# Kernel optimization log

Measured on AMD Instinct MI355X. Metric: run time of the kernel, lower is better.

Reference implementation:

```python
import jax, jax.numpy as jnp
import numpy as np

B, S, H, D = 2, 2048, 16, 64
DM = H * D  # d_model = 1024


def setup_inputs() -> dict:
    key = jax.random.key(0)
    ks = jax.random.split(key, 12)
    scale = 1.0 / np.sqrt(DM)
    inp = {
        "queries": jax.random.normal(ks[0], (B, S, DM), jnp.float32),
        "keys": jax.random.normal(ks[1], (B, S, DM), jnp.float32),
        "values": jax.random.normal(ks[2], (B, S, DM), jnp.float32),
        # binary (0/1) causal mask, broadcast to (B, H, S, S) as the torch API expects
        "mask": jnp.broadcast_to(jnp.tril(jnp.ones((S, S), jnp.float32)), (B, H, S, S)),
        "wq": jax.random.normal(ks[3], (DM, DM), jnp.float32) * scale,
        "bq": jax.random.normal(ks[4], (DM,), jnp.float32) * scale,
        "wk": jax.random.normal(ks[5], (DM, DM), jnp.float32) * scale,
        "bk": jax.random.normal(ks[6], (DM,), jnp.float32) * scale,
        "wv": jax.random.normal(ks[7], (DM, DM), jnp.float32) * scale,
        "bv": jax.random.normal(ks[8], (DM,), jnp.float32) * scale,
        "wy": jax.random.normal(ks[9], (DM, DM), jnp.float32) * scale,
        "by": jax.random.normal(ks[10], (DM,), jnp.float32) * scale,
    }
    return inp


def _split_heads(x):
    # (B, S, H*D) -> (B, H, S, D)
    b, s, _ = x.shape
    return x.reshape(b, s, H, D).transpose(0, 2, 1, 3)


def reference(queries, keys, values, mask, wq, bq, wk, bk, wv, bv, wy, by):
    # torch nn.Linear: y = x @ W^T + b
    q = _split_heads(queries @ wq.T + bq)  # (B, H, S, D)
    k = _split_heads(keys @ wk.T + bk)
    v = _split_heads(values @ wv.T + bv)

    s = jnp.einsum("bhqd,bhkd->bhqk", q, k) / jnp.sqrt(jnp.float32(D))
    # custom additive-multiplicative mask: s*mask - 1e4*(1-mask)
    s = s * mask - 1e4 * (1.0 - mask)
    w = jax.nn.softmax(s, axis=-1)
    av = jnp.einsum("bhqk,bhkd->bhqd", w, v)  # (B, H, S, D)
    y = av.transpose(0, 2, 1, 3).reshape(queries.shape[0], queries.shape[1], DM)
    return y @ wy.T + by
```

## Files before the change

kernel.cpp:

```cpp
#include <hip/hip_runtime.h>
#include <math.h>

#define BB 2
#define SS 2048
#define HH 16
#define DD 64
#define DMODEL 1024
#define MROWS (BB * SS)

typedef __attribute__((ext_vector_type(8))) short bf16x8;
typedef __attribute__((ext_vector_type(4))) float f32x4;

__device__ __forceinline__ f32x4 mfma16(bf16x8 a, bf16x8 b, f32x4 c) {
    return __builtin_amdgcn_mfma_f32_16x16x32_bf16(a, b, c, 0, 0, 0);
}

__device__ __forceinline__ unsigned short bf16_1(float x) {
    unsigned u = __builtin_bit_cast(unsigned, x);
    u += 0x7fffu + ((u >> 16) & 1u);
    return (unsigned short)(u >> 16);
}
__device__ __forceinline__ unsigned pack_bf16(float a, float b) {
    unsigned ua = __builtin_bit_cast(unsigned, a);
    unsigned ub = __builtin_bit_cast(unsigned, b);
    ua += 0x7fffu + ((ua >> 16) & 1u);
    ub += 0x7fffu + ((ub >> 16) & 1u);
    return (ua >> 16) | (ub & 0xffff0000u);
}

__global__ __launch_bounds__(256) void cvt_bf16(const float* __restrict__ q,
                                                const float* __restrict__ k,
                                                const float* __restrict__ v,
                                                const float* __restrict__ wq,
                                                const float* __restrict__ wk,
                                                const float* __restrict__ wv,
                                                const float* __restrict__ wy,
                                                unsigned short* __restrict__ dst)
{
    const size_t idx = ((size_t)blockIdx.x * 256 + threadIdx.x) * 8;
    const int mc = (int)(idx >> 20);
    const float* src; size_t off;
    if      (mc < 4)   { src = q;  off = idx; }
    else if (mc < 8)   { src = k;  off = idx - ((size_t)4  << 20); }
    else if (mc < 12)  { src = v;  off = idx - ((size_t)8  << 20); }
    else if (mc == 12) { src = wq; off = idx - ((size_t)12 << 20); }
    else if (mc == 13) { src = wk; off = idx - ((size_t)13 << 20); }
    else if (mc == 14) { src = wv; off = idx - ((size_t)14 << 20); }
    else               { src = wy; off = idx - ((size_t)15 << 20); }
    float4 a = *(const float4*)(src + off);
    float4 b = *(const float4*)(src + off + 4);
    uint4 o;
    o.x = pack_bf16(a.x, a.y); o.y = pack_bf16(a.z, a.w);
    o.z = pack_bf16(b.x, b.y); o.w = pack_bf16(b.z, b.w);
    *(uint4*)(dst + idx) = o;
}

__global__ __launch_bounds__(256) void gemm_mfma(const unsigned short* __restrict__ A,
                                                 const unsigned short* __restrict__ W,
                                                 const float* __restrict__ bias,
                                                 void* __restrict__ out,
                                                 int a_mode, int out_mode)
{
    __shared__ int4 lds4[2048];
    const int tid = threadIdx.x;
    const int w   = tid >> 6;
    const int lane = tid & 63;
    const int L = lane & 15, Q = lane >> 4;
    const int m0 = blockIdx.x * 128;
    const int n0 = blockIdx.y * 128;
    const int wm = (w & 1) * 64;
    const int wn = (w >> 1) * 64;

    f32x4 acc[4][4] = {};

    for (int c = 0; c < 16; ++c) {
        __syncthreads();
        #pragma unroll
        for (int i = 0; i < 4; ++i) {
            int cid = tid + 256 * i;
            int row = cid >> 3, ch = cid & 7;
            int m = m0 + row;
            size_t gaddr;
            if (a_mode == 0) gaddr = (size_t)m * DMODEL + (size_t)c * 64 + ch * 8;
            else {
                int b = m >> 11, s = m & 2047;
                gaddr = (((size_t)b * HH + c) * SS + s) * DD + ch * 8;
            }
            int4 val = *(const int4*)(A + gaddr);
            lds4[row * 8 + (ch ^ (row & 7))] = val;
        }
        #pragma unroll
        for (int i = 0; i < 4; ++i) {
            int cid = tid + 256 * i;
            int row = cid >> 3, ch = cid & 7;
            int4 val = *(const int4*)(W + (size_t)(n0 + row) * DMODEL + (size_t)c * 64 + ch * 8);
            lds4[1024 + row * 8 + (ch ^ (row & 7))] = val;
        }
        __syncthreads();
        #pragma unroll
        for (int kf = 0; kf < 2; ++kf) {
            bf16x8 af[4], bfr[4];
            #pragma unroll
            for (int mt = 0; mt < 4; ++mt) {
                int row = wm + 16 * mt + L;
                af[mt] = __builtin_bit_cast(bf16x8, lds4[row * 8 + ((Q + 4 * kf) ^ (L & 7))]);
            }
            #pragma unroll
            for (int nt = 0; nt < 4; ++nt) {
                int row = wn + 16 * nt + L;
                bfr[nt] = __builtin_bit_cast(bf16x8, lds4[1024 + row * 8 + ((Q + 4 * kf) ^ (L & 7))]);
            }
            #pragma unroll
            for (int mt = 0; mt < 4; ++mt)
                #pragma unroll
                for (int nt = 0; nt < 4; ++nt)
                    acc[mt][nt] = mfma16(af[mt], bfr[nt], acc[mt][nt]);
        }
    }

    #pragma unroll
    for (int mt = 0; mt < 4; ++mt)
        #pragma unroll
        for (int nt = 0; nt < 4; ++nt)
            #pragma unroll
            for (int r = 0; r < 4; ++r) {
                int m = m0 + wm + 16 * mt + 4 * Q + r;
                int n = n0 + wn + 16 * nt + L;
                float val = acc[mt][nt][r] + bias[n];
                if (out_mode == 0) {
                    int b = m >> 11, s = m & 2047, h = n >> 6, d = n & 63;
                    ((unsigned short*)out)[(((size_t)b * HH + h) * SS + s) * DD + d] = bf16_1(val);
                } else {
                    ((float*)out)[(size_t)m * DMODEL + n] = val;
                }
            }
}

__global__ __launch_bounds__(256) void attn_mfma(const unsigned short* __restrict__ qb,
                                                 const unsigned short* __restrict__ kb,
                                                 const unsigned short* __restrict__ vb,
                                                 unsigned short* __restrict__ av)
{
    __shared__ int4 lds4[2048];
    const int tid  = threadIdx.x;
    const int w    = tid >> 6;
    const int lane = tid & 63;
    const int L = lane & 15, Q = lane >> 4;
    const int h = blockIdx.y, b = blockIdx.z;
    const size_t base = ((size_t)b * HH + h) * SS * DD;
    const float SC = 0.125f * 1.4426950408889634f;

    const int srcA = L + 32 * (Q & 1);
    const int srcB = srcA + 16;

    for (int pass = 0; pass < 2; ++pass) {
        const int qt  = pass ? (15 - (int)blockIdx.x) : (int)blockIdx.x;
        const int q0  = qt * 128;
        const int q0w = q0 + 32 * w;

        __syncthreads();
        #pragma unroll
        for (int i = 0; i < 4; ++i) {
            int cid = tid + 256 * i;
            int row = cid >> 3, ch = cid & 7;
            int4 val = *(const int4*)(qb + base + (size_t)(q0 + row) * DD + ch * 8);
            lds4[row * 8 + (ch ^ (row & 7))] = val;
        }
        __syncthreads();

        bf16x8 qf[2][2];
        #pragma unroll
        for (int ct = 0; ct < 2; ++ct)
            #pragma unroll
            for (int kf = 0; kf < 2; ++kf) {
                int row = 32 * w + 16 * ct + L;
                qf[ct][kf] = __builtin_bit_cast(bf16x8, lds4[row * 8 + ((Q + 4 * kf) ^ (L & 7))]);
            }

        float m2[2] = {-1e30f, -1e30f};
        float l2[2] = {0.f, 0.f};
        f32x4 acc[4][2] = {};

        const int nkt   = 2 * qt + 2;
        const int qmaxw = q0w + 31;
        for (int kt = 0; kt < nkt; ++kt) {
            const int k0 = kt * 64;
            __syncthreads();
            #pragma unroll
            for (int i = 0; i < 2; ++i) {
                int cid = tid + 256 * i;
                int row = cid >> 3, ch = cid & 7;
                int4 val = *(const int4*)(kb + base + (size_t)(k0 + row) * DD + ch * 8);
                lds4[1024 + row * 8 + (ch ^ (row & 7))] = val;
            }
            {
                int r4 = tid >> 4, c4 = tid & 15;
                uint2 rv[4];
                #pragma unroll
                for (int i = 0; i < 4; ++i)
                    rv[i] = *(const uint2*)(vb + base + (size_t)(k0 + r4 * 4 + i) * DD + c4 * 4);
                uint2* vt2 = (uint2*)(lds4 + 1536);
                #pragma unroll
                for (int j = 0; j < 4; ++j) {
                    int vrow = c4 * 4 + j;
                    unsigned e0 = ((j < 2 ? rv[0].x : rv[0].y) >> ((j & 1) * 16)) & 0xffffu;
                    unsigned e1 = ((j < 2 ? rv[1].x : rv[1].y) >> ((j & 1) * 16)) & 0xffffu;
                    unsigned e2 = ((j < 2 ? rv[2].x : rv[2].y) >> ((j & 1) * 16)) & 0xffffu;
                    unsigned e3 = ((j < 2 ? rv[3].x : rv[3].y) >> ((j & 1) * 16)) & 0xffffu;
                    uint2 wv2; wv2.x = e0 | (e1 << 16); wv2.y = e2 | (e3 << 16);
                    int ch = (r4 >> 1) ^ (vrow & 7);
                    vt2[(vrow * 8 + ch) * 2 + (r4 & 1)] = wv2;
                }
            }
            __syncthreads();

            if (k0 <= qmaxw) {
                f32x4 st[4][2] = {};
                #pragma unroll
                for (int kf = 0; kf < 2; ++kf) {
                    bf16x8 kfr[4];
                    #pragma unroll
                    for (int rt = 0; rt < 4; ++rt) {
                        int row = 16 * rt + L;
                        kfr[rt] = __builtin_bit_cast(bf16x8, lds4[1024 + row * 8 + ((Q + 4 * kf) ^ (L & 7))]);
                    }
                    #pragma unroll
                    for (int rt = 0; rt < 4; ++rt)
                        #pragma unroll
                        for (int ct = 0; ct < 2; ++ct)
                            st[rt][ct] = mfma16(kfr[rt], qf[ct][kf], st[rt][ct]);
                }
                const bool need_mask = (k0 + 63 > q0w);
                unsigned pd[4][2][2];
                #pragma unroll
                for (int ct = 0; ct < 2; ++ct) {
                    const int qg = q0w + 16 * ct + L;
                    float mx = -1e30f;
                    #pragma unroll
                    for (int rt = 0; rt < 4; ++rt)
                        #pragma unroll
                        for (int r = 0; r < 4; ++r) {
                            float s = st[rt][ct][r] * SC;
                            if (need_mask) {
                                int kg = k0 + 16 * rt + 4 * Q + r;
                                s = (kg > qg) ? -2e30f : s;
                            }
                            st[rt][ct][r] = s;
                            mx = fmaxf(mx, s);
                        }
                    mx = fmaxf(mx, __shfl_xor(mx, 16, 64));
                    mx = fmaxf(mx, __shfl_xor(mx, 32, 64));
                    float mn = fmaxf(m2[ct], mx);
                    float alpha = exp2f(m2[ct] - mn);
                    m2[ct] = mn;
                    float ls = 0.f;
                    #pragma unroll
                    for (int rt = 0; rt < 4; ++rt) {
                        #pragma unroll
                        for (int r = 0; r < 4; ++r) {
                            float p = exp2f(st[rt][ct][r] - mn);
                            st[rt][ct][r] = p;
                            ls += p;
                        }
                        pd[rt][ct][0] = pack_bf16(st[rt][ct][0], st[rt][ct][1]);
                        pd[rt][ct][1] = pack_bf16(st[rt][ct][2], st[rt][ct][3]);
                    }
                    ls += __shfl_xor(ls, 16, 64);
                    ls += __shfl_xor(ls, 32, 64);
                    l2[ct] = l2[ct] * alpha + ls;
                    #pragma unroll
                    for (int rt = 0; rt < 4; ++rt)
                        acc[rt][ct] *= alpha;
                }
                #pragma unroll
                for (int kf = 0; kf < 2; ++kf) {
                    bf16x8 vf[4];
                    #pragma unroll
                    for (int rt = 0; rt < 4; ++rt) {
                        int row = 16 * rt + L;
                        vf[rt] = __builtin_bit_cast(bf16x8, lds4[1536 + row * 8 + ((Q + 4 * kf) ^ (L & 7))]);
                    }
                    #pragma unroll
                    for (int ct = 0; ct < 2; ++ct) {
                        unsigned lo0 = pd[2 * kf + 0][ct][0], lo1 = pd[2 * kf + 0][ct][1];
                        unsigned hi0 = pd[2 * kf + 1][ct][0], hi1 = pd[2 * kf + 1][ct][1];
                        unsigned xa_lo0 = (unsigned)__shfl((int)lo0, srcA, 64);
                        unsigned xa_lo1 = (unsigned)__shfl((int)lo1, srcA, 64);
                        unsigned xb_lo0 = (unsigned)__shfl((int)lo0, srcB, 64);
                        unsigned xb_lo1 = (unsigned)__shfl((int)lo1, srcB, 64);
                        unsigned xa_hi0 = (unsigned)__shfl((int)hi0, srcA, 64);
                        unsigned xa_hi1 = (unsigned)__shfl((int)hi1, srcA, 64);
                        unsigned xb_hi0 = (unsigned)__shfl((int)hi0, srcB, 64);
                        unsigned xb_hi1 = (unsigned)__shfl((int)hi1, srcB, 64);
                        const bool hisel = (Q & 2) != 0;
                        uint4 bw;
                        bw.x = hisel ? xa_hi0 : xa_lo0;
                        bw.y = hisel ? xa_hi1 : xa_lo1;
                        bw.z = hisel ? xb_hi0 : xb_lo0;
                        bw.w = hisel ? xb_hi1 : xb_lo1;
                        bf16x8 pf = __builtin_bit_cast(bf16x8, bw);
                        #pragma unroll
                        for (int rt = 0; rt < 4; ++rt)
                            acc[rt][ct] = mfma16(vf[rt], pf, acc[rt][ct]);
                    }
                }
            }
        }

        __syncthreads();
        {
            int4* ep4 = lds4 + w * 512;
            float inv0 = 1.0f / l2[0], inv1 = 1.0f / l2[1];
            #pragma unroll
            for (int ct = 0; ct < 2; ++ct) {
                int qr = 16 * ct + L;
                float inv = ct ? inv1 : inv0;
                #pragma unroll
                for (int rt = 0; rt < 4; ++rt) {
                    f32x4 ov = acc[rt][ct] * inv;
                    ep4[qr * 16 + ((4 * rt + Q) ^ (qr & 15))] = __builtin_bit_cast(int4, ov);
                }
            }
        }
        __syncthreads();
        {
            uint2* epu = (uint2*)(lds4 + w * 512);
            #pragma unroll
            for (int i = 0; i < 16; ++i) {
                int pid = lane + 64 * i;
                int rr  = pid >> 5;
                int c   = pid & 31;
                uint2 f2 = epu[(rr * 16 + ((c >> 1) ^ (rr & 15))) * 2 + (c & 1)];
                unsigned packed = pack_bf16(__builtin_bit_cast(float, f2.x),
                                            __builtin_bit_cast(float, f2.y));
                *(unsigned*)(av + base + (size_t)(q0 + 32 * w + rr) * DD + c * 2) = packed;
            }
        }
    }
}

extern "C" void kernel_launch(void* const* d_in, const int* in_sizes, int n_in,
                              void* d_out, int out_size, void* d_ws, size_t ws_size,
                              hipStream_t stream) {
    const float* queries = (const float*)d_in[0];
    const float* keys    = (const float*)d_in[1];
    const float* values  = (const float*)d_in[2];
    const float* wq = (const float*)d_in[4];
    const float* bq = (const float*)d_in[5];
    const float* wk = (const float*)d_in[6];
    const float* bk = (const float*)d_in[7];
    const float* wv = (const float*)d_in[8];
    const float* bv = (const float*)d_in[9];
    const float* wy = (const float*)d_in[10];
    const float* by = (const float*)d_in[11];

    unsigned short* wsb = (unsigned short*)d_ws;
    const size_t M4 = (size_t)1 << 22, M1 = (size_t)1 << 20;
    unsigned short* qcv = wsb;
    unsigned short* kcv = qcv + M4;
    unsigned short* vcv = kcv + M4;
    unsigned short* wqb = vcv + M4;
    unsigned short* wkb = wqb + M1;
    unsigned short* wvb = wkb + M1;
    unsigned short* wyb = wvb + M1;
    unsigned short* qh  = wyb + M1;
    unsigned short* kh  = qh + M4;
    unsigned short* vh  = kh + M4;
    unsigned short* avb = vh + M4;

    cvt_bf16<<<8192, 256, 0, stream>>>(queries, keys, values, wq, wk, wv, wy, qcv);

    dim3 ggrid(MROWS / 128, DMODEL / 128);
    gemm_mfma<<<ggrid, 256, 0, stream>>>(qcv, wqb, bq, qh, 0, 0);
    gemm_mfma<<<ggrid, 256, 0, stream>>>(kcv, wkb, bk, kh, 0, 0);
    gemm_mfma<<<ggrid, 256, 0, stream>>>(vcv, wvb, bv, vh, 0, 0);

    attn_mfma<<<dim3(8, HH, BB), 256, 0, stream>>>(qh, kh, vh, avb);

    gemm_mfma<<<ggrid, 256, 0, stream>>>(avb, wyb, by, d_out, 1, 1);
}
```

Measured before the change: 848.6 us.

## Fuse QKV GEMMs, emit transposed V, shrink attention and output tiles

The three projection GEMMs become one launch with a z-dimension selecting Q/K/V. The V projection now writes V transposed directly in its epilogue, so the attention kernel no longer transposes V in registers each key tile. Attention moves to 64-row query tiles (16 rows per wave) with twice as many blocks, and the output GEMM uses 64-row tiles to double its block count. The aim is better occupancy and less per-tile overhead, at the cost of less reuse of K/V per block and strided 8-byte stores in the V epilogue.

```diff
diff --git a/kernel.cpp b/kernel.cpp
--- a/kernel.cpp
+++ b/kernel.cpp
@@ -55,28 +55,30 @@
     *(uint4*)(dst + idx) = o;
 }
 
-__global__ __launch_bounds__(256) void gemm_mfma(const unsigned short* __restrict__ A,
-                                                 const unsigned short* __restrict__ W,
-                                                 const float* __restrict__ bias,
-                                                 void* __restrict__ out,
-                                                 int a_mode, int out_mode)
-{
-    __shared__ int4 lds4[2048];
+template<int TM>
+__device__ __forceinline__ void gemm_body(const unsigned short* __restrict__ A,
+                                          const unsigned short* __restrict__ W,
+                                          const float* __restrict__ bias,
+                                          void* __restrict__ out,
+                                          int a_mode, int out_mode)
+{
+    constexpr int NT  = (TM == 128) ? 4 : 2;
+    constexpr int ACH = TM * 8;
+    __shared__ int4 lds4[ACH + 1024];
     const int tid = threadIdx.x;
-    const int w   = tid >> 6;
-    const int lane = tid & 63;
+    const int w = tid >> 6, lane = tid & 63;
     const int L = lane & 15, Q = lane >> 4;
-    const int m0 = blockIdx.x * 128;
+    const int m0 = blockIdx.x * TM;
     const int n0 = blockIdx.y * 128;
-    const int wm = (w & 1) * 64;
-    const int wn = (w >> 1) * 64;
-
-    f32x4 acc[4][4] = {};
+    const int wm = (TM == 128) ? (w & 1) * 64 : 0;
+    const int wn = (TM == 128) ? (w >> 1) * 64 : w * 32;
+
+    f32x4 acc[4][NT] = {};
 
     for (int c = 0; c < 16; ++c) {
         __syncthreads();
         #pragma unroll
-        for (int i = 0; i < 4; ++i) {
+        for (int i = 0; i < TM / 32; ++i) {
             int cid = tid + 256 * i;
             int row = cid >> 3, ch = cid & 7;
             int m = m0 + row;
@@ -86,34 +88,33 @@
                 int b = m >> 11, s = m & 2047;
                 gaddr = (((size_t)b * HH + c) * SS + s) * DD + ch * 8;
             }
-            int4 val = *(const int4*)(A + gaddr);
-            lds4[row * 8 + (ch ^ (row & 7))] = val;
+            lds4[row * 8 + (ch ^ (row & 7))] = *(const int4*)(A + gaddr);
         }
         #pragma unroll
         for (int i = 0; i < 4; ++i) {
             int cid = tid + 256 * i;
             int row = cid >> 3, ch = cid & 7;
-            int4 val = *(const int4*)(W + (size_t)(n0 + row) * DMODEL + (size_t)c * 64 + ch * 8);
-            lds4[1024 + row * 8 + (ch ^ (row & 7))] = val;
+            lds4[ACH + row * 8 + (ch ^ (row & 7))] =
+                *(const int4*)(W + (size_t)(n0 + row) * DMODEL + (size_t)c * 64 + ch * 8);
         }
         __syncthreads();
         #pragma unroll
         for (int kf = 0; kf < 2; ++kf) {
-            bf16x8 af[4], bfr[4];
+            bf16x8 af[4], bfr[NT];
             #pragma unroll
             for (int mt = 0; mt < 4; ++mt) {
                 int row = wm + 16 * mt + L;
-                af[mt] = __builtin_bit_cast(bf16x8, lds4[row * 8 + ((Q + 4 * kf) ^ (L & 7))]);
-            }
-            #pragma unroll
-            for (int nt = 0; nt < 4; ++nt) {
+                af[mt] = __builtin_bit_cast(bf16x8, lds4[row * 8 + ((Q + 4 * kf) ^ (row & 7))]);
+            }
+            #pragma unroll
+            for (int nt = 0; nt < NT; ++nt) {
                 int row = wn + 16 * nt + L;
-                bfr[nt] = __builtin_bit_cast(bf16x8, lds4[1024 + row * 8 + ((Q + 4 * kf) ^ (L & 7))]);
+                bfr[nt] = __builtin_bit_cast(bf16x8, lds4[ACH + row * 8 + ((Q + 4 * kf) ^ (row & 7))]);
             }
             #pragma unroll
             for (int mt = 0; mt < 4; ++mt)
                 #pragma unroll
-                for (int nt = 0; nt < 4; ++nt)
+                for (int nt = 0; nt < NT; ++nt)
                     acc[mt][nt] = mfma16(af[mt], bfr[nt], acc[mt][nt]);
         }
     }
@@ -121,27 +122,63 @@
     #pragma unroll
     for (int mt = 0; mt < 4; ++mt)
         #pragma unroll
-        for (int nt = 0; nt < 4; ++nt)
-            #pragma unroll
-            for (int r = 0; r < 4; ++r) {
-                int m = m0 + wm + 16 * mt + 4 * Q + r;
-                int n = n0 + wn + 16 * nt + L;
-                float val = acc[mt][nt][r] + bias[n];
-                if (out_mode == 0) {
-                    int b = m >> 11, s = m & 2047, h = n >> 6, d = n & 63;
-                    ((unsigned short*)out)[(((size_t)b * HH + h) * SS + s) * DD + d] = bf16_1(val);
-                } else {
-                    ((float*)out)[(size_t)m * DMODEL + n] = val;
-                }
-            }
+        for (int nt = 0; nt < NT; ++nt) {
+            const int mbase = m0 + wm + 16 * mt + 4 * Q;
+            const int n = n0 + wn + 16 * nt + L;
+            float v0 = acc[mt][nt][0] + bias[n];
+            float v1 = acc[mt][nt][1] + bias[n];
+            float v2 = acc[mt][nt][2] + bias[n];
+            float v3 = acc[mt][nt][3] + bias[n];
+            if (out_mode == 1) {
+                float* o = (float*)out + (size_t)mbase * DMODEL + n;
+                o[0] = v0; o[DMODEL] = v1; o[2 * DMODEL] = v2; o[3 * DMODEL] = v3;
+            } else if (out_mode == 0) {
+                int b = mbase >> 11, s = mbase & 2047, h = n >> 6, d = n & 63;
+                unsigned short* o = (unsigned short*)out + (((size_t)b * HH + h) * SS + s) * DD + d;
+                o[0] = bf16_1(v0); o[DD] = bf16_1(v1); o[2 * DD] = bf16_1(v2); o[3 * DD] = bf16_1(v3);
+            } else {
+                int b = mbase >> 11, s = mbase & 2047, h = n >> 6, d = n & 63;
+                uint2 p; p.x = pack_bf16(v0, v1); p.y = pack_bf16(v2, v3);
+                *(uint2*)((unsigned short*)out + (((size_t)b * HH + h) * DD + d) * SS + s) = p;
+            }
+        }
+}
+
+__global__ __launch_bounds__(256) void qkv_gemm(const unsigned short* __restrict__ qcv,
+                                                const unsigned short* __restrict__ kcv,
+                                                const unsigned short* __restrict__ vcv,
+                                                const unsigned short* __restrict__ wqb,
+                                                const unsigned short* __restrict__ wkb,
+                                                const unsigned short* __restrict__ wvb,
+                                                const float* __restrict__ bq,
+                                                const float* __restrict__ bk,
+                                                const float* __restrict__ bv,
+                                                unsigned short* __restrict__ qh,
+                                                unsigned short* __restrict__ kh,
+                                                unsigned short* __restrict__ vtb)
+{
+    const int z = blockIdx.z;
+    const unsigned short* A = (z == 0) ? qcv : (z == 1) ? kcv : vcv;
+    const unsigned short* W = (z == 0) ? wqb : (z == 1) ? wkb : wvb;
+    const float* bias       = (z == 0) ? bq  : (z == 1) ? bk  : bv;
+    unsigned short* out     = (z == 0) ? qh  : (z == 1) ? kh  : vtb;
+    gemm_body<128>(A, W, bias, out, 0, (z == 2) ? 2 : 0);
+}
+
+__global__ __launch_bounds__(256) void out_gemm(const unsigned short* __restrict__ avb,
+                                                const unsigned short* __restrict__ wyb,
+                                                const float* __restrict__ by,
+                                                float* __restrict__ out)
+{
+    gemm_body<64>(avb, wyb, by, out, 1, 1);
 }
 
 __global__ __launch_bounds__(256) void attn_mfma(const unsigned short* __restrict__ qb,
                                                  const unsigned short* __restrict__ kb,
-                                                 const unsigned short* __restrict__ vb,
+                                                 const unsigned short* __restrict__ vt,
                                                  unsigned short* __restrict__ av)
 {
-    __shared__ int4 lds4[2048];
+    __shared__ int4 lds4[1536];
     const int tid  = threadIdx.x;
     const int w    = tid >> 6;
     const int lane = tid & 63;
@@ -152,37 +189,34 @@
 
     const int srcA = L + 32 * (Q & 1);
     const int srcB = srcA + 16;
+    const bool hisel = (Q & 2) != 0;
 
     for (int pass = 0; pass < 2; ++pass) {
-        const int qt  = pass ? (15 - (int)blockIdx.x) : (int)blockIdx.x;
-        const int q0  = qt * 128;
-        const int q0w = q0 + 32 * w;
-
-        __syncthreads();
-        #pragma unroll
-        for (int i = 0; i < 4; ++i) {
+        const int qt  = pass ? (31 - (int)blockIdx.x) : (int)blockIdx.x;
+        const int q0  = qt * 64;
+        const int q0w = q0 + 16 * w;
+
+        __syncthreads();
+        #pragma unroll
+        for (int i = 0; i < 2; ++i) {
             int cid = tid + 256 * i;
             int row = cid >> 3, ch = cid & 7;
-            int4 val = *(const int4*)(qb + base + (size_t)(q0 + row) * DD + ch * 8);
-            lds4[row * 8 + (ch ^ (row & 7))] = val;
-        }
-        __syncthreads();
-
-        bf16x8 qf[2][2];
-        #pragma unroll
-        for (int ct = 0; ct < 2; ++ct)
-            #pragma unroll
-            for (int kf = 0; kf < 2; ++kf) {
-                int row = 32 * w + 16 * ct + L;
-                qf[ct][kf] = __builtin_bit_cast(bf16x8, lds4[row * 8 + ((Q + 4 * kf) ^ (L & 7))]);
-            }
-
-        float m2[2] = {-1e30f, -1e30f};
-        float l2[2] = {0.f, 0.f};
-        f32x4 acc[4][2] = {};
-
-        const int nkt   = 2 * qt + 2;
-        const int qmaxw = q0w + 31;
+            lds4[row * 8 + (ch ^ (row & 7))] =
+                *(const int4*)(qb + base + (size_t)(q0 + row) * DD + ch * 8);
+        }
+        __syncthreads();
+
+        bf16x8 qf[2];
+        #pragma unroll
+        for (int kf = 0; kf < 2; ++kf) {
+            int row = 16 * w + L;
+            qf[kf] = __builtin_bit_cast(bf16x8, lds4[row * 8 + ((Q + 4 * kf) ^ (row & 7))]);
+        }
+
+        float m2 = -1e30f, l2 = 0.f;
+        f32x4 acc[4] = {};
+
+        const int nkt = qt + 1;
         for (int kt = 0; kt < nkt; ++kt) {
             const int k0 = kt * 64;
             __syncthreads();
@@ -190,150 +224,120 @@
             for (int i = 0; i < 2; ++i) {
                 int cid = tid + 256 * i;
                 int row = cid >> 3, ch = cid & 7;
-                int4 val = *(const int4*)(kb + base + (size_t)(k0 + row) * DD + ch * 8);
-                lds4[1024 + row * 8 + (ch ^ (row & 7))] = val;
-            }
-            {
-                int r4 = tid >> 4, c4 = tid & 15;
-                uint2 rv[4];
-                #pragma unroll
-                for (int i = 0; i < 4; ++i)
-                    rv[i] = *(const uint2*)(vb + base + (size_t)(k0 + r4 * 4 + i) * DD + c4 * 4);
-                uint2* vt2 = (uint2*)(lds4 + 1536);
-                #pragma unroll
-                for (int j = 0; j < 4; ++j) {
-                    int vrow = c4 * 4 + j;
-                    unsigned e0 = ((j < 2 ? rv[0].x : rv[0].y) >> ((j & 1) * 16)) & 0xffffu;
-                    unsigned e1 = ((j < 2 ? rv[1].x : rv[1].y) >> ((j & 1) * 16)) & 0xffffu;
-                    unsigned e2 = ((j < 2 ? rv[2].x : rv[2].y) >> ((j & 1) * 16)) & 0xffffu;
-                    unsigned e3 = ((j < 2 ? rv[3].x : rv[3].y) >> ((j & 1) * 16)) & 0xffffu;
-                    uint2 wv2; wv2.x = e0 | (e1 << 16); wv2.y = e2 | (e3 << 16);
-                    int ch = (r4 >> 1) ^ (vrow & 7);
-                    vt2[(vrow * 8 + ch) * 2 + (r4 & 1)] = wv2;
+                lds4[512 + row * 8 + (ch ^ (row & 7))] =
+                    *(const int4*)(kb + base + (size_t)(k0 + row) * DD + ch * 8);
+            }
+            #pragma unroll
+            for (int i = 0; i < 2; ++i) {
+                int cid = tid + 256 * i;
+                int row = cid >> 3, ch = cid & 7;
+                lds4[1024 + row * 8 + (ch ^ (row & 7))] =
+                    *(const int4*)(vt + base + (size_t)row * SS + k0 + ch * 8);
+            }
+            __syncthreads();
+
+            f32x4 st[4] = {};
+            #pragma unroll
+            for (int kf = 0; kf < 2; ++kf) {
+                bf16x8 kfr[4];
+                #pragma unroll
+                for (int rt = 0; rt < 4; ++rt) {
+                    int row = 16 * rt + L;
+                    kfr[rt] = __builtin_bit_cast(bf16x8, lds4[512 + row * 8 + ((Q + 4 * kf) ^ (row & 7))]);
                 }
-            }
-            __syncthreads();
-
-            if (k0 <= qmaxw) {
-                f32x4 st[4][2] = {};
-                #pragma unroll
-                for (int kf = 0; kf < 2; ++kf) {
-                    bf16x8 kfr[4];
-                    #pragma unroll
-                    for (int rt = 0; rt < 4; ++rt) {
-                        int row = 16 * rt + L;
-                        kfr[rt] = __builtin_bit_cast(bf16x8, lds4[1024 + row * 8 + ((Q + 4 * kf) ^ (L & 7))]);
+                #pragma unroll
+                for (int rt = 0; rt < 4; ++rt)
+                    st[rt] = mfma16(kfr[rt], qf[kf], st[rt]);
+            }
+
+            const bool need_mask = (k0 + 63 > q0w);
+            const int qg = q0w + L;
+            float mx = -1e30f;
+            #pragma unroll
+            for (int rt = 0; rt < 4; ++rt)
+                #pragma unroll
+                for (int r = 0; r < 4; ++r) {
+                    float s = st[rt][r] * SC;
+                    if (need_mask) {
+                        int kg = k0 + 16 * rt + 4 * Q + r;
+                        s = (kg > qg) ? -2e30f : s;
                     }
-                    #pragma unroll
-                    for (int rt = 0; rt < 4; ++rt)
-                        #pragma unroll
-                        for (int ct = 0; ct < 2; ++ct)
-                            st[rt][ct] = mfma16(kfr[rt], qf[ct][kf], st[rt][ct]);
+                    st[rt][r] = s;
+                    mx = fmaxf(mx, s);
                 }
-                const bool need_mask = (k0 + 63 > q0w);
-                unsigned pd[4][2][2];
-                #pragma unroll
-                for (int ct = 0; ct < 2; ++ct) {
-                    const int qg = q0w + 16 * ct + L;
-                    float mx = -1e30f;
-                    #pragma unroll
-                    for (int rt = 0; rt < 4; ++rt)
-                        #pragma unroll
-                        for (int r = 0; r < 4; ++r) {
-                            float s = st[rt][ct][r] * SC;
-                            if (need_mask) {
-                                int kg = k0 + 16 * rt + 4 * Q + r;
-                                s = (kg > qg) ? -2e30f : s;
-                            }
-                            st[rt][ct][r] = s;
-                            mx = fmaxf(mx, s);
-                        }
-                    mx = fmaxf(mx, __shfl_xor(mx, 16, 64));
-                    mx = fmaxf(mx, __shfl_xor(mx, 32, 64));
-                    float mn = fmaxf(m2[ct], mx);
-                    float alpha = exp2f(m2[ct] - mn);
-                    m2[ct] = mn;
-                    float ls = 0.f;
-                    #pragma unroll
-                    for (int rt = 0; rt < 4; ++rt) {
-                        #pragma unroll
-                        for (int r = 0; r < 4; ++r) {
-                            float p = exp2f(st[rt][ct][r] - mn);
-                            st[rt][ct][r] = p;
-                            ls += p;
-                        }
-                        pd[rt][ct][0] = pack_bf16(st[rt][ct][0], st[rt][ct][1]);
-                        pd[rt][ct][1] = pack_bf16(st[rt][ct][2], st[rt][ct][3]);
-                    }
-                    ls += __shfl_xor(ls, 16, 64);
-                    ls += __shfl_xor(ls, 32, 64);
-                    l2[ct] = l2[ct] * alpha + ls;
-                    #pragma unroll
-                    for (int rt = 0; rt < 4; ++rt)
-                        acc[rt][ct] *= alpha;
+            mx = fmaxf(mx, __shfl_xor(mx, 16, 64));
+            mx = fmaxf(mx, __shfl_xor(mx, 32, 64));
+            const float mn = fmaxf(m2, mx);
+            const float alpha = exp2f(m2 - mn);
+            m2 = mn;
+            float ls = 0.f;
+            unsigned pd[4][2];
+            #pragma unroll
+            for (int rt = 0; rt < 4; ++rt) {
+                float p0 = exp2f(st[rt][0] - mn), p1 = exp2f(st[rt][1] - mn);
+                float p2 = exp2f(st[rt][2] - mn), p3 = exp2f(st[rt][3] - mn);
+                ls += (p0 + p1) + (p2 + p3);
+                pd[rt][0] = pack_bf16(p0, p1);
+                pd[rt][1] = pack_bf16(p2, p3);
+            }
+            ls += __shfl_xor(ls, 16, 64);
+            ls += __shfl_xor(ls, 32, 64);
+            l2 = l2 * alpha + ls;
+            #pragma unroll
+            for (int rt = 0; rt < 4; ++rt) acc[rt] *= alpha;
+
+            #pragma unroll
+            for (int kf = 0; kf < 2; ++kf) {
+                bf16x8 vf[4];
+                #pragma unroll
+                for (int rt = 0; rt < 4; ++rt) {
+                    int row = 16 * rt + L;
+                    vf[rt] = __builtin_bit_cast(bf16x8, lds4[1024 + row * 8 + ((Q + 4 * kf) ^ (row & 7))]);
                 }
-                #pragma unroll
-                for (int kf = 0; kf < 2; ++kf) {
-                    bf16x8 vf[4];
-                    #pragma unroll
-                    for (int rt = 0; rt < 4; ++rt) {
-                        int row = 16 * rt + L;
-                        vf[rt] = __builtin_bit_cast(bf16x8, lds4[1536 + row * 8 + ((Q + 4 * kf) ^ (L & 7))]);
-                    }
-                    #pragma unroll
-                    for (int ct = 0; ct < 2; ++ct) {
-                        unsigned lo0 = pd[2 * kf + 0][ct][0], lo1 = pd[2 * kf + 0][ct][1];
-                        unsigned hi0 = pd[2 * kf + 1][ct][0], hi1 = pd[2 * kf + 1][ct][1];
-                        unsigned xa_lo0 = (unsigned)__shfl((int)lo0, srcA, 64);
-                        unsigned xa_lo1 = (unsigned)__shfl((int)lo1, srcA, 64);
-                        unsigned xb_lo0 = (unsigned)__shfl((int)lo0, srcB, 64);
-                        unsigned xb_lo1 = (unsigned)__shfl((int)lo1, srcB, 64);
-                        unsigned xa_hi0 = (unsigned)__shfl((int)hi0, srcA, 64);
-                        unsigned xa_hi1 = (unsigned)__shfl((int)hi1, srcA, 64);
-                        unsigned xb_hi0 = (unsigned)__shfl((int)hi0, srcB, 64);
-                        unsigned xb_hi1 = (unsigned)__shfl((int)hi1, srcB, 64);
-                        const bool hisel = (Q & 2) != 0;
-                        uint4 bw;
-                        bw.x = hisel ? xa_hi0 : xa_lo0;
-                        bw.y = hisel ? xa_hi1 : xa_lo1;
-                        bw.z = hisel ? xb_hi0 : xb_lo0;
-                        bw.w = hisel ? xb_hi1 : xb_lo1;
-                        bf16x8 pf = __builtin_bit_cast(bf16x8, bw);
-                        #pragma unroll
-                        for (int rt = 0; rt < 4; ++rt)
-                            acc[rt][ct] = mfma16(vf[rt], pf, acc[rt][ct]);
-                    }
-                }
+                unsigned lo0 = pd[2 * kf + 0][0], lo1 = pd[2 * kf + 0][1];
+                unsigned hi0 = pd[2 * kf + 1][0], hi1 = pd[2 * kf + 1][1];
+                unsigned xa_lo0 = (unsigned)__shfl((int)lo0, srcA, 64);
+                unsigned xa_lo1 = (unsigned)__shfl((int)lo1, srcA, 64);
+                unsigned xb_lo0 = (unsigned)__shfl((int)lo0, srcB, 64);
+                unsigned xb_lo1 = (unsigned)__shfl((int)lo1, srcB, 64);
+                unsigned xa_hi0 = (unsigned)__shfl((int)hi0, srcA, 64);
+                unsigned xa_hi1 = (unsigned)__shfl((int)hi1, srcA, 64);
+                unsigned xb_hi0 = (unsigned)__shfl((int)hi0, srcB, 64);
+                unsigned xb_hi1 = (unsigned)__shfl((int)hi1, srcB, 64);
+                uint4 bw;
+                bw.x = hisel ? xa_hi0 : xa_lo0;
+                bw.y = hisel ? xa_hi1 : xa_lo1;
+                bw.z = hisel ? xb_hi0 : xb_lo0;
+                bw.w = hisel ? xb_hi1 : xb_lo1;
+                bf16x8 pf = __builtin_bit_cast(bf16x8, bw);
+                #pragma unroll
+                for (int rt = 0; rt < 4; ++rt)
+                    acc[rt] = mfma16(vf[rt], pf, acc[rt]);
             }
         }
 
         __syncthreads();
         {
-            int4* ep4 = lds4 + w * 512;
-            float inv0 = 1.0f / l2[0], inv1 = 1.0f / l2[1];
-            #pragma unroll
-            for (int ct = 0; ct < 2; ++ct) {
-                int qr = 16 * ct + L;
-                float inv = ct ? inv1 : inv0;
-                #pragma unroll
-                for (int rt = 0; rt < 4; ++rt) {
-                    f32x4 ov = acc[rt][ct] * inv;
-                    ep4[qr * 16 + ((4 * rt + Q) ^ (qr & 15))] = __builtin_bit_cast(int4, ov);
-                }
+            int4* ep4 = lds4 + w * 256;
+            const float inv = 1.0f / l2;
+            #pragma unroll
+            for (int rt = 0; rt < 4; ++rt) {
+                f32x4 ov = acc[rt] * inv;
+                ep4[L * 16 + ((4 * rt + Q) ^ (L & 15))] = __builtin_bit_cast(int4, ov);
             }
         }
         __syncthreads();
         {
-            uint2* epu = (uint2*)(lds4 + w * 512);
-            #pragma unroll
-            for (int i = 0; i < 16; ++i) {
+            uint2* epu = (uint2*)(lds4 + w * 256);
+            #pragma unroll
+            for (int i = 0; i < 8; ++i) {
                 int pid = lane + 64 * i;
                 int rr  = pid >> 5;
                 int c   = pid & 31;
                 uint2 f2 = epu[(rr * 16 + ((c >> 1) ^ (rr & 15))) * 2 + (c & 1)];
                 unsigned packed = pack_bf16(__builtin_bit_cast(float, f2.x),
                                             __builtin_bit_cast(float, f2.y));
-                *(unsigned*)(av + base + (size_t)(q0 + 32 * w + rr) * DD + c * 2) = packed;
+                *(unsigned*)(av + base + (size_t)(q0 + 16 * w + rr) * DD + c * 2) = packed;
             }
         }
     }
@@ -365,17 +369,15 @@
     unsigned short* wyb = wvb + M1;
     unsigned short* qh  = wyb + M1;
     unsigned short* kh  = qh + M4;
-    unsigned short* vh  = kh + M4;
-    unsigned short* avb = vh + M4;
+    unsigned short* vtb = kh + M4;
+    unsigned short* avb = vtb + M4;
 
     cvt_bf16<<<8192, 256, 0, stream>>>(queries, keys, values, wq, wk, wv, wy, qcv);
 
-    dim3 ggrid(MROWS / 128, DMODEL / 128);
-    gemm_mfma<<<ggrid, 256, 0, stream>>>(qcv, wqb, bq, qh, 0, 0);
-    gemm_mfma<<<ggrid, 256, 0, stream>>>(kcv, wkb, bk, kh, 0, 0);
-    gemm_mfma<<<ggrid, 256, 0, stream>>>(vcv, wvb, bv, vh, 0, 0);
-
-    attn_mfma<<<dim3(8, HH, BB), 256, 0, stream>>>(qh, kh, vh, avb);
-
-    gemm_mfma<<<ggrid, 256, 0, stream>>>(avb, wyb, by, d_out, 1, 1);
-}
+    qkv_gemm<<<dim3(MROWS / 128, DMODEL / 128, 3), 256, 0, stream>>>(
+        qcv, kcv, vcv, wqb, wkb, wvb, bq, bk, bv, qh, kh, vtb);
+
+    attn_mfma<<<dim3(16, HH, BB), 256, 0, stream>>>(qh, kh, vtb, avb);
+
+    out_gemm<<<dim3(MROWS / 64, DMODEL / 128), 256, 0, stream>>>(avb, wyb, by, (float*)d_out);
+}
```

After: 748.6 us. -11.8%, faster.
